# Kernel tuning notes

Measured on AMD Instinct MI355X. Metric: run time of the kernel, lower is better.

Reference implementation:

```python
import jax, jax.numpy as jnp
import numpy as np

GROUP_SIZE = 128  # K-rows sharing one dequant scale


def _dequant(B, s):
    """Unpack int4 (uint4b8: value = nibble - 8) from packed int32 and apply group scales.
    B: [K//8, N] int32, 8 nibbles per word along K (nibble i -> k = 8*row + i).
    s: [K//GROUP_SIZE, N] float scales.
    Returns W: [K, N] float.
    """
    Kp, N = B.shape
    K = Kp * 8
    shifts = (jnp.arange(8, dtype=jnp.int32) * 4)
    # [Kp, 8, N] nibbles -> [K, N]
    nib = (B[:, None, :] >> shifts[None, :, None]) & 0xF
    w = nib.reshape(K, N).astype(s.dtype) - 8.0
    # per-group scaling: groups of GROUP_SIZE consecutive K rows
    w = (w.reshape(K // GROUP_SIZE, GROUP_SIZE, N) * s[:, None, :]).reshape(K, N)
    return w


def setup_inputs() -> dict:
    key = jax.random.key(0)
    k1, k2, k3 = jax.random.split(key, 3)
    M, K, N = 64, 8192, 8192
    x = jax.random.normal(k1, (M, K), dtype=jnp.float32)
    B = jax.random.randint(k2, (K // 8, N), 0, 2147483647, dtype=jnp.int32)
    s = jax.random.uniform(k3, (K // GROUP_SIZE, N), dtype=jnp.float32) * 0.02
    return {"x": x, "B": B, "s": s}


def reference(x, B, s):
    # machete_mm: fused int4 dequant + GEMM; here expressed as dequant then matmul
    w = _dequant(B, s)          # [K, N]
    out = x @ w                 # [M, N]
    return out
```

## Files before the change

### kernel.cpp

```cpp
#include <hip/hip_runtime.h>

typedef _Float16 half2v __attribute__((ext_vector_type(2)));
typedef _Float16 half8  __attribute__((ext_vector_type(8)));
typedef float    floatx4 __attribute__((ext_vector_type(4)));

#define M_DIM 64
#define K_DIM 8192
#define N_DIM 8192
#define NT 64
#define KSB 4

__global__ __launch_bounds__(256) void permute_x_kernel(
        const float* __restrict__ x, _Float16* __restrict__ xp) {
    int t = blockIdx.x * 256 + threadIdx.x;
    const float* src = x + (size_t)t * 8;
    float4 a = *(const float4*)(src);
    float4 b = *(const float4*)(src + 4);
    union { _Float16 h[8]; float4 f; } u;
    u.h[0] = (_Float16)a.x; u.h[1] = (_Float16)b.x;
    u.h[2] = (_Float16)a.y; u.h[3] = (_Float16)b.y;
    u.h[4] = (_Float16)a.z; u.h[5] = (_Float16)b.z;
    u.h[6] = (_Float16)a.w; u.h[7] = (_Float16)b.w;
    *(float4*)(xp + (size_t)t * 8) = u.f;
}

__device__ __forceinline__ half2v dq_pair(unsigned int bits, half2v sub, half2v sc) {
    union { unsigned int u; half2v h; } cv;
    cv.u = bits;
    return (cv.h - sub) * sc;
}

__global__ __launch_bounds__(256, 2) void machete_mm_kernel(
        const _Float16* __restrict__ xp,
        const unsigned int* __restrict__ Bq,
        const float* __restrict__ s,
        float* __restrict__ partial) {
    __shared__ float red[4][32][65];

    const int tid  = threadIdx.x;
    const int w    = tid >> 6;
    const int lane = tid & 63;
    const int c    = lane & 15;
    const int q    = lane >> 4;
    const int n0   = blockIdx.x * NT;
    const int ci   = blockIdx.y * 4 + w;
    const int kb   = ci * (K_DIM / (KSB * 4));

    const int ncol = n0 + 4 * c;

    floatx4 acc[4][4];
    #pragma unroll
    for (int i = 0; i < 4; ++i)
        #pragma unroll
        for (int j = 0; j < 4; ++j) acc[i][j] = (floatx4)0.0f;

    const half2v c1032 = { (_Float16)1032.0f, (_Float16)1032.0f };
    half2v s2g[4][4];
    #pragma unroll
    for (int g = 0; g < 4; ++g) {
        const float4 s4 = *(const float4*)(s + (size_t)((kb >> 7) + g) * N_DIM + ncol);
        s2g[g][0] = (half2v){ (_Float16)s4.x, (_Float16)s4.x };
        s2g[g][1] = (half2v){ (_Float16)s4.y, (_Float16)s4.y };
        s2g[g][2] = (half2v){ (_Float16)s4.z, (_Float16)s4.z };
        s2g[g][3] = (half2v){ (_Float16)s4.w, (_Float16)s4.w };
    }

    const unsigned int* bptr = Bq + (size_t)((kb >> 3) + q) * N_DIM + ncol;
    const _Float16*     aptr = xp + (size_t)c * K_DIM + kb + q * 8;

    uint4 bbuf[3];
    half8 abuf[2][4];
    bbuf[0] = *(const uint4*)bptr; bptr += (size_t)4 * N_DIM;
    bbuf[1] = *(const uint4*)bptr; bptr += (size_t)4 * N_DIM;
    #pragma unroll
    for (int mt = 0; mt < 4; ++mt)
        abuf[0][mt] = *(const half8*)(aptr + (size_t)mt * 16 * K_DIM);

    #pragma unroll
    for (int st = 0; st < 16; ++st) {
        if (st < 14) {
            bbuf[(st + 2) % 3] = *(const uint4*)bptr;
            bptr += (size_t)4 * N_DIM;
        }
        if (st < 15) {
            #pragma unroll
            for (int mt = 0; mt < 4; ++mt)
                abuf[(st + 1) & 1][mt] =
                    *(const half8*)(aptr + 32 + (size_t)mt * 16 * K_DIM);
        }

        union { uint4 v; unsigned int a[4]; } bv;
        bv.v = bbuf[st % 3];
        const int g = st >> 2;

        #pragma unroll
        for (int t = 0; t < 4; ++t) {
            const unsigned int wd = bv.a[t];
            const half2v sc = s2g[g][t];
            union { half2v h2[4]; half8 h8; } bf;
            bf.h2[0] = dq_pair(( wd        & 0x000F000Fu) | 0x64006400u, c1032, sc);
            bf.h2[1] = dq_pair(((wd >> 4)  & 0x000F000Fu) | 0x64006400u, c1032, sc);
            bf.h2[2] = dq_pair(((wd >> 8)  & 0x000F000Fu) | 0x64006400u, c1032, sc);
            bf.h2[3] = dq_pair(((wd >> 12) & 0x000F000Fu) | 0x64006400u, c1032, sc);
            #pragma unroll
            for (int mt = 0; mt < 4; ++mt)
                acc[mt][t] = __builtin_amdgcn_mfma_f32_16x16x32_f16(
                    abuf[st & 1][mt], bf.h8, acc[mt][t], 0, 0, 0);
        }
        aptr += 32;
    }

    float* ptile = partial + ((size_t)blockIdx.y * M_DIM) * N_DIM + n0;
    #pragma unroll
    for (int r = 0; r < 2; ++r) {
        if (r) __syncthreads();
        #pragma unroll
        for (int h = 0; h < 2; ++h) {
            const int mt = 2 * r + h;
            #pragma unroll
            for (int t = 0; t < 4; ++t)
                #pragma unroll
                for (int rr = 0; rr < 4; ++rr)
                    red[w][h * 16 + q * 4 + rr][4 * c + t] = acc[mt][t][rr];
        }
        __syncthreads();
        #pragma unroll
        for (int i = 0; i < 8; ++i) {
            const int idx = i * 256 + tid;
            const int mr  = idx >> 6;
            const int nl  = idx & 63;
            const float v = red[0][mr][nl] + red[1][mr][nl]
                          + red[2][mr][nl] + red[3][mr][nl];
            ptile[(size_t)(r * 32 + mr) * N_DIM + nl] = v;
        }
    }
}

__global__ __launch_bounds__(256) void reduce_kernel(
        const float* __restrict__ partial, float* __restrict__ out) {
    const size_t i = ((size_t)blockIdx.x * 256 + threadIdx.x) * 4;
    const size_t S = (size_t)M_DIM * N_DIM;
    float4 v = *(const float4*)(partial + i);
    #pragma unroll
    for (int bk = 1; bk < KSB; ++bk) {
        const float4 u = *(const float4*)(partial + bk * S + i);
        v.x += u.x; v.y += u.y; v.z += u.z; v.w += u.w;
    }
    *(float4*)(out + i) = v;
}

extern "C" void kernel_launch(void* const* d_in, const int* in_sizes, int n_in,
                              void* d_out, int out_size, void* d_ws, size_t ws_size,
                              hipStream_t stream) {
    const float*        x  = (const float*)d_in[0];
    const unsigned int* Bq = (const unsigned int*)d_in[1];
    const float*        sc = (const float*)d_in[2];
    float* out     = (float*)d_out;
    _Float16* xp   = (_Float16*)d_ws;
    float* partial = (float*)((char*)d_ws + (1 << 20));

    permute_x_kernel<<<dim3((M_DIM * K_DIM / 8) / 256), 256, 0, stream>>>(x, xp);
    machete_mm_kernel<<<dim3(N_DIM / NT, KSB), 256, 0, stream>>>(xp, Bq, sc, partial);
    reduce_kernel<<<dim3(M_DIM * N_DIM / (256 * 4)), 256, 0, stream>>>(partial, out);
}
```

Before: 104.2 us.

## Double split-K, retile x into fragment-order layout, restructure pipeline loop

Doubles the split-K factor so each wave handles a shorter K chunk and the grid has twice as many blocks, and raises the occupancy hint to three blocks per SM. x is now rearranged into MFMA fragment order so each lane loads contiguous half8 values. The main loop is rolled (unroll 2) with a two-deep B buffer, and all four B fragments are dequantised before the MFMAs are issued. The cost is twice as much partial-sum traffic and a heavier reduce kernel, plus less prefetch depth for B.

```diff
diff --git a/kernel.cpp b/kernel.cpp
--- a/kernel.cpp
+++ b/kernel.cpp
@@ -8,12 +8,20 @@
 #define K_DIM 8192
 #define N_DIM 8192
 #define NT 64
-#define KSB 4
+#define KSB 8
+#define CHUNK (K_DIM / (KSB * 4))
+#define STEPS (CHUNK / 32)
 
 __global__ __launch_bounds__(256) void permute_x_kernel(
         const float* __restrict__ x, _Float16* __restrict__ xp) {
-    int t = blockIdx.x * 256 + threadIdx.x;
-    const float* src = x + (size_t)t * 8;
+    const int t  = blockIdx.x * 256 + threadIdx.x;
+    const int c  = t & 15;
+    const int q  = (t >> 4) & 3;
+    const int mt = (t >> 6) & 3;
+    const int kb = t >> 8;
+    const int m  = mt * 16 + c;
+    const int k0 = kb * 32 + q * 8;
+    const float* src = x + (size_t)m * K_DIM + k0;
     float4 a = *(const float4*)(src);
     float4 b = *(const float4*)(src + 4);
     union { _Float16 h[8]; float4 f; } u;
@@ -30,7 +38,7 @@
     return (cv.h - sub) * sc;
 }
 
-__global__ __launch_bounds__(256, 2) void machete_mm_kernel(
+__global__ __launch_bounds__(256, 3) void machete_mm_kernel(
         const _Float16* __restrict__ xp,
         const unsigned int* __restrict__ Bq,
         const float* __restrict__ s,
@@ -44,8 +52,7 @@
     const int q    = lane >> 4;
     const int n0   = blockIdx.x * NT;
     const int ci   = blockIdx.y * 4 + w;
-    const int kb   = ci * (K_DIM / (KSB * 4));
-
+    const int kb   = ci * CHUNK;
     const int ncol = n0 + 4 * c;
 
     floatx4 acc[4][4];
@@ -55,9 +62,9 @@
         for (int j = 0; j < 4; ++j) acc[i][j] = (floatx4)0.0f;
 
     const half2v c1032 = { (_Float16)1032.0f, (_Float16)1032.0f };
-    half2v s2g[4][4];
+    half2v s2g[2][4];
     #pragma unroll
-    for (int g = 0; g < 4; ++g) {
+    for (int g = 0; g < 2; ++g) {
         const float4 s4 = *(const float4*)(s + (size_t)((kb >> 7) + g) * N_DIM + ncol);
         s2g[g][0] = (half2v){ (_Float16)s4.x, (_Float16)s4.x };
         s2g[g][1] = (half2v){ (_Float16)s4.y, (_Float16)s4.y };
@@ -65,49 +72,52 @@
         s2g[g][3] = (half2v){ (_Float16)s4.w, (_Float16)s4.w };
     }
 
-    const unsigned int* bptr = Bq + (size_t)((kb >> 3) + q) * N_DIM + ncol;
-    const _Float16*     aptr = xp + (size_t)c * K_DIM + kb + q * 8;
+    const unsigned int* bq = Bq + (size_t)((kb >> 3) + q) * N_DIM + ncol;
+    const _Float16*     ap = xp + (size_t)(kb >> 5) * 2048 + lane * 8;
 
-    uint4 bbuf[3];
+    uint4 bbuf[2];
     half8 abuf[2][4];
-    bbuf[0] = *(const uint4*)bptr; bptr += (size_t)4 * N_DIM;
-    bbuf[1] = *(const uint4*)bptr; bptr += (size_t)4 * N_DIM;
+    bbuf[0] = *(const uint4*)bq; bq += (size_t)4 * N_DIM;
+    bbuf[1] = *(const uint4*)bq; bq += (size_t)4 * N_DIM;
     #pragma unroll
     for (int mt = 0; mt < 4; ++mt)
-        abuf[0][mt] = *(const half8*)(aptr + (size_t)mt * 16 * K_DIM);
+        abuf[0][mt] = *(const half8*)(ap + mt * 512);
 
-    #pragma unroll
-    for (int st = 0; st < 16; ++st) {
-        if (st < 14) {
-            bbuf[(st + 2) % 3] = *(const uint4*)bptr;
-            bptr += (size_t)4 * N_DIM;
-        }
-        if (st < 15) {
-            #pragma unroll
-            for (int mt = 0; mt < 4; ++mt)
-                abuf[(st + 1) & 1][mt] =
-                    *(const half8*)(aptr + 32 + (size_t)mt * 16 * K_DIM);
-        }
+    #pragma unroll 2
+    for (int st = 0; st < STEPS; ++st) {
+        const int p = st & 1;
+        const int g = st >> 2;
 
         union { uint4 v; unsigned int a[4]; } bv;
-        bv.v = bbuf[st % 3];
-        const int g = st >> 2;
-
+        bv.v = bbuf[p];
+        half8 bf[4];
         #pragma unroll
         for (int t = 0; t < 4; ++t) {
             const unsigned int wd = bv.a[t];
             const half2v sc = s2g[g][t];
-            union { half2v h2[4]; half8 h8; } bf;
-            bf.h2[0] = dq_pair(( wd        & 0x000F000Fu) | 0x64006400u, c1032, sc);
-            bf.h2[1] = dq_pair(((wd >> 4)  & 0x000F000Fu) | 0x64006400u, c1032, sc);
-            bf.h2[2] = dq_pair(((wd >> 8)  & 0x000F000Fu) | 0x64006400u, c1032, sc);
-            bf.h2[3] = dq_pair(((wd >> 12) & 0x000F000Fu) | 0x64006400u, c1032, sc);
+            union { half2v h2[4]; half8 h8; } b8;
+            b8.h2[0] = dq_pair(( wd        & 0x000F000Fu) | 0x64006400u, c1032, sc);
+            b8.h2[1] = dq_pair(((wd >> 4)  & 0x000F000Fu) | 0x64006400u, c1032, sc);
+            b8.h2[2] = dq_pair(((wd >> 8)  & 0x000F000Fu) | 0x64006400u, c1032, sc);
+            b8.h2[3] = dq_pair(((wd >> 12) & 0x000F000Fu) | 0x64006400u, c1032, sc);
+            bf[t] = b8.h8;
+        }
+
+        if (st < STEPS - 2) bbuf[p] = *(const uint4*)bq;
+        bq += (size_t)4 * N_DIM;
+        if (st < STEPS - 1) {
+            ap += 2048;
+            #pragma unroll
+            for (int mt = 0; mt < 4; ++mt)
+                abuf[p ^ 1][mt] = *(const half8*)(ap + mt * 512);
+        }
+
+        #pragma unroll
+        for (int t = 0; t < 4; ++t)
             #pragma unroll
             for (int mt = 0; mt < 4; ++mt)
                 acc[mt][t] = __builtin_amdgcn_mfma_f32_16x16x32_f16(
-                    abuf[st & 1][mt], bf.h8, acc[mt][t], 0, 0, 0);
-        }
-        aptr += 32;
+                    abuf[p][mt], bf[t], acc[mt][t], 0, 0, 0);
     }
 
     float* ptile = partial + ((size_t)blockIdx.y * M_DIM) * N_DIM + n0;
@@ -159,7 +169,7 @@
     _Float16* xp   = (_Float16*)d_ws;
     float* partial = (float*)((char*)d_ws + (1 << 20));
 
-    permute_x_kernel<<<dim3((M_DIM * K_DIM / 8) / 256), 256, 0, stream>>>(x, xp);
+    permute_x_kernel<<<dim3(M_DIM * K_DIM / 8 / 256), 256, 0, stream>>>(x, xp);
     machete_mm_kernel<<<dim3(N_DIM / NT, KSB), 256, 0, stream>>>(xp, Bq, sc, partial);
     reduce_kernel<<<dim3(M_DIM * N_DIM / (256 * 4)), 256, 0, stream>>>(partial, out);
 }
```

Result: faster. 100.4 us (-3.6%).
